# Kernel tuning notes

Hardware: AMD Instinct MI355X
Metric: run time of the kernel (lower is better)

## Reference

```python
import jax, jax.numpy as jnp
import numpy as np

THRESHOLD = 1.0  # CIF firing threshold (init kwarg)


def setup_inputs() -> dict:
    key = jax.random.key(0)
    k1, k2 = jax.random.split(key)
    B, T, H = 32, 2048, 512
    return {
        "hidden": jax.random.normal(k1, (B, T, H), dtype=jnp.float32),
        "alphas": jax.random.uniform(k2, (B, T), dtype=jnp.float32),
        "integrate": jnp.zeros((B,), dtype=jnp.float32),
        "frame": jnp.zeros((B, H), dtype=jnp.float32),
    }


def cif_scan(hidden, alphas, integrate, frame, threshold):
    """Continuous integrate-and-fire recurrence over time, vectorized over batch.

    hidden: [B,T,H], alphas: [B,T], integrate: [B], frame: [B,H]
    Returns fires [B,T], frames [B,T,H], integrate_new [B], frame_new [B,H].
    """

    def step(carry, inp):
        integ, fr = carry          # [B], [B,H]
        alpha, h_t = inp           # [B], [B,H]
        dist_completion = 1.0 - integ
        integ = integ + alpha
        fire = integ >= threshold                       # [B] bool
        integ_next = jnp.where(fire, integ - 1.0, integ)
        cur = jnp.where(fire, dist_completion, alpha)   # weight spent this step
        rem = alpha - cur                               # leftover weight after firing
        fr_out = fr + cur[:, None] * h_t                # frame recorded at this step
        fr_next = jnp.where(fire[:, None], rem[:, None] * h_t, fr_out)
        return (integ_next, fr_next), (integ, fr_out)

    xs = (jnp.swapaxes(alphas, 0, 1), jnp.swapaxes(hidden, 0, 1))  # time-major
    (integ_f, frame_f), (fires_t, frames_t) = jax.lax.scan(step, (integrate, frame), xs)
    fires = jnp.swapaxes(fires_t, 0, 1)    # [B,T]
    frames = jnp.swapaxes(frames_t, 0, 1)  # [B,T,H]
    return fires, frames, integ_f, frame_f


def reference(hidden, alphas, integrate, frame):
    T = hidden.shape[1]
    fires, frames, integ_new, frame_new = cif_scan(hidden, alphas, integrate, frame, THRESHOLD)
    # torch.index_select(frames[0], 0, nonzero(fires[0] >= threshold)) -> data-dependent
    # shape; emulate with jit-safe padded nonzero (padding rows replicate row 0).
    idx = jnp.nonzero(fires[0] >= THRESHOLD, size=T, fill_value=0)[0]
    frame_sel = frames[0][idx]  # [T, H], first num_fires rows are the fired frames
    return frame_sel, integ_new, frame_new
```

## Files before the change

### kernel.cpp

```cpp
#include <hip/hip_runtime.h>


#define THRESH 1.0f
#define MAX_T 4096
#define MAX_CH 64

__device__ __forceinline__ float fract_exact(float x) {
    float r; asm("v_fract_f32 %0, %1" : "=v"(r) : "v"(x)); return r;
}

__global__ __launch_bounds__(256) void cif_transpose_kernel(
    const float4* __restrict__ a4, float4* __restrict__ aT4, int B, int T4)
{
    int tid = blockIdx.x * blockDim.x + threadIdx.x;
    if (tid >= B * T4) return;
    int b = tid / T4, c = tid - b * T4;
    aT4[(size_t)c * B + b] = a4[tid];
}

__global__ __launch_bounds__(64) void cif_chain_kernel(
    const float4* __restrict__ aT4,
    const float*  __restrict__ integ0,
    float* __restrict__ chunkInteg,
    float* __restrict__ integ_out,
    int B, int T)
{
    const int lane = threadIdx.x;
    const bool act = lane < B;
    const int nchunk = T >> 6;
    float integ = act ? integ0[lane] : 0.0f;
    float4 bufA[16], bufB[16];

#define LOADCH(buf, c) do { if (act) { \
    _Pragma("unroll") for (int j = 0; j < 16; ++j) \
        buf[j] = aT4[(size_t)((c) * 16 + j) * B + lane]; } } while (0)

#define DOCH(buf, c) do { if (act) { \
    chunkInteg[(size_t)(c) * B + lane] = integ; \
    _Pragma("unroll") for (int j = 0; j < 16; ++j) { \
        integ = fract_exact(integ + buf[j].x); \
        integ = fract_exact(integ + buf[j].y); \
        integ = fract_exact(integ + buf[j].z); \
        integ = fract_exact(integ + buf[j].w); \
    } } } while (0)

    LOADCH(bufA, 0);
    for (int c = 0; c < nchunk; c += 2) {
        if (c + 1 < nchunk) LOADCH(bufB, c + 1);
        DOCH(bufA, c);
        if (c + 2 < nchunk) LOADCH(bufA, c + 2);
        if (c + 1 < nchunk) DOCH(bufB, c + 1);
    }
#undef LOADCH
#undef DOCH

    if (act) integ_out[lane] = integ;
}

__global__ __launch_bounds__(1024) void cif_replay_kernel(
    const float4* __restrict__ aT4,
    const float*  __restrict__ chunkInteg,
    float* __restrict__ gT,
    int* __restrict__ rowStart, int* __restrict__ rowEnd, int* __restrict__ rowFlags,
    int* __restrict__ tlast,
    int B, int T)
{
    const int nchunk = T >> 6;
    const int tid = threadIdx.x;
    __shared__ unsigned long long s_mask[2048];
    __shared__ int s_fire[MAX_T];
    __shared__ int s_nf, s_f0;

    if (tid < nchunk * B) {
        const int c = tid / B, b = tid - c * B;
        float integ = chunkInteg[tid];
        unsigned long long m = 0;
        for (int j = 0; j < 16; ++j) {
            const float4 a4 = aT4[(size_t)(c * 16 + j) * B + b];
            const float av[4] = {a4.x, a4.y, a4.z, a4.w};
            float gv[4];
#pragma unroll
            for (int k = 0; k < 4; ++k) {
                const int idx = j * 4 + k;
                const float alpha = av[k];
                const float s   = integ + alpha;
                const bool fire = (s >= THRESH);
                const float sm1 = s - 1.0f;
                integ = fire ? sm1 : s;
                gv[k] = fire ? sm1 : alpha;
                m |= fire ? (1ull << idx) : 0ull;
            }
#pragma unroll
            for (int k = 0; k < 4; ++k)
                gT[(size_t)(c * 64 + j * 4 + k) * B + b] = gv[k];
        }
        s_mask[tid] = m;
    }
    __syncthreads();

    if (tid < B) {
        int tl = -1;
        for (int c = nchunk - 1; c >= 0; --c) {
            const unsigned long long mc = s_mask[c * B + tid];
            if (mc) { tl = c * 64 + 63 - __clzll(mc); break; }
        }
        tlast[tid] = tl;
    }

    if (tid < 64) {
        unsigned long long m0 = (tid < nchunk) ? s_mask[tid * B] : 0ull;
        const int pc = __popcll(m0);
        int x = pc;
#pragma unroll
        for (int d = 1; d < 64; d <<= 1) {
            const int y = __shfl_up(x, d);
            if (tid >= d) x += y;
        }
        if (tid == 63) s_nf = x;
        if (tid == 0)  s_f0 = (int)(m0 & 1ull);
        int r = x - pc;
        while (m0) {
            const int p = __ffsll(m0) - 1;
            s_fire[r++] = tid * 64 + p;
            m0 &= m0 - 1;
        }
    }
    __syncthreads();

    const int nf = s_nf, f0 = s_f0;
    for (int r = tid; r < T; r += blockDim.x) {
        int st, en, fl;
        if (r < nf) {
            en = s_fire[r];
            st = (r == 0) ? 0 : s_fire[r - 1];
            fl = ((r == 0) ? 1 : 0) | 2;
        } else {
            st = 0; en = 0; fl = 1 | (f0 ? 2 : 0);
        }
        rowStart[r] = st; rowEnd[r] = en; rowFlags[r] = fl;
    }
}

__global__ __launch_bounds__(128) void cif_out_kernel(
    const float* __restrict__ hidden,
    const float* __restrict__ frame0,
    const float* __restrict__ gT,
    const float* __restrict__ alphas,
    const int* __restrict__ rowStart, const int* __restrict__ rowEnd,
    const int* __restrict__ rowFlags, const int* __restrict__ tlast,
    float* __restrict__ out_sel,
    float* __restrict__ frame_out,
    int B, int T, int H)
{
    const int blk = blockIdx.x;

    if (blk < T) {
        const int r = blk;
        const int start = rowStart[r], end = rowEnd[r], fl = rowFlags[r];
        const float a  = alphas[end];
        const float ge = gT[(size_t)end * B];
        const float wend = (fl & 2) ? (a - ge) : a;
        for (int h0 = threadIdx.x * 4; h0 < H; h0 += 128 * 4) {
            float4 acc = (fl & 1) ? *reinterpret_cast<const float4*>(frame0 + h0)
                                  : make_float4(0.f, 0.f, 0.f, 0.f);
            for (int s = start; s < end; ++s) {
                const float  w  = gT[(size_t)s * B];
                const float4 hv = *reinterpret_cast<const float4*>(hidden + (size_t)s * H + h0);
                acc.x += w * hv.x; acc.y += w * hv.y;
                acc.z += w * hv.z; acc.w += w * hv.w;
            }
            const float4 hv = *reinterpret_cast<const float4*>(hidden + (size_t)end * H + h0);
            acc.x += wend * hv.x; acc.y += wend * hv.y;
            acc.z += wend * hv.z; acc.w += wend * hv.w;
            *reinterpret_cast<float4*>(out_sel + (size_t)r * H + h0) = acc;
        }
    } else {
        const int b  = blk - T;
        const int tl = tlast[b];
        const int start = (tl < 0) ? 0 : tl;
        const float* hb = hidden + (size_t)b * T * H;
        for (int h0 = threadIdx.x * 4; h0 < H; h0 += 128 * 4) {
            float4 acc = (tl < 0) ? *reinterpret_cast<const float4*>(frame0 + (size_t)b * H + h0)
                                  : make_float4(0.f, 0.f, 0.f, 0.f);
            for (int s = start; s < T; ++s) {
                const float  w  = gT[(size_t)s * B + b];
                const float4 hv = *reinterpret_cast<const float4*>(hb + (size_t)s * H + h0);
                acc.x += w * hv.x; acc.y += w * hv.y;
                acc.z += w * hv.z; acc.w += w * hv.w;
            }
            *reinterpret_cast<float4*>(frame_out + (size_t)b * H + h0) = acc;
        }
    }
}

extern "C" void kernel_launch(void* const* d_in, const int* in_sizes, int n_in,
                              void* d_out, int out_size, void* d_ws, size_t ws_size,
                              hipStream_t stream) {
    const float* hidden    = (const float*)d_in[0];
    const float* alphas    = (const float*)d_in[1];
    const float* integrate = (const float*)d_in[2];
    const float* frame     = (const float*)d_in[3];

    const int B = in_sizes[2];
    const int T = in_sizes[1] / B;
    const int H = in_sizes[3] / B;

    float* out       = (float*)d_out;
    float* out_sel   = out;
    float* integ_out = out + (size_t)T * H;
    float* frame_out = integ_out + B;

    char* ws = (char*)d_ws;
    float4* aT4       = (float4*)ws;  ws += sizeof(float) * (size_t)B * T;
    float*  gT        = (float*)ws;   ws += sizeof(float) * (size_t)B * T;
    float*  chunkInteg= (float*)ws;   ws += sizeof(float) * (size_t)(T / 64) * B;
    int* rowStart = (int*)ws;         ws += sizeof(int) * T;
    int* rowEnd   = (int*)ws;         ws += sizeof(int) * T;
    int* rowFlags = (int*)ws;         ws += sizeof(int) * T;
    int* tlast    = (int*)ws;         ws += sizeof(int) * B;

    const int T4 = T / 4;
    cif_transpose_kernel<<<(B * T4 + 255) / 256, 256, 0, stream>>>(
        (const float4*)alphas, aT4, B, T4);

    cif_chain_kernel<<<1, 64, 0, stream>>>(
        aT4, integrate, chunkInteg, integ_out, B, T);

    cif_replay_kernel<<<1, 1024, 0, stream>>>(
        aT4, chunkInteg, gT, rowStart, rowEnd, rowFlags, tlast, B, T);

    cif_out_kernel<<<T + B, 128, 0, stream>>>(
        hidden, frame, gT, alphas, rowStart, rowEnd, rowFlags, tlast,
        out_sel, frame_out, B, T, H);
}
```

Baseline: 206.8 us.

## Fuse transpose, chain and replay kernels into one single-block prep kernel

Merges the alpha transpose, the chunk-level integrate chain and the per-chunk replay into one 512-thread single-block kernel. Chunk start values now stay in shared memory instead of a global buffer. This removes two kernel launches and their inter-kernel gaps. In exchange, the transpose that previously ran across many blocks is now done by a single block, and the replay loop runs with 512 threads instead of 1024, so it needs two passes.

```diff
diff --git a/kernel.cpp b/kernel.cpp
--- a/kernel.cpp
+++ b/kernel.cpp
@@ -2,82 +2,78 @@
 
 
 #define THRESH 1.0f
-#define MAX_T 4096
-#define MAX_CH 64
+#define MAXB   64
+#define MAXT   2048
+#define MAXCH  (MAXT / 64)
 
 __device__ __forceinline__ float fract_exact(float x) {
     float r; asm("v_fract_f32 %0, %1" : "=v"(r) : "v"(x)); return r;
 }
 
-__global__ __launch_bounds__(256) void cif_transpose_kernel(
-    const float4* __restrict__ a4, float4* __restrict__ aT4, int B, int T4)
-{
-    int tid = blockIdx.x * blockDim.x + threadIdx.x;
-    if (tid >= B * T4) return;
-    int b = tid / T4, c = tid - b * T4;
-    aT4[(size_t)c * B + b] = a4[tid];
-}
-
-__global__ __launch_bounds__(64) void cif_chain_kernel(
-    const float4* __restrict__ aT4,
+__global__ __launch_bounds__(512) void cif_prep_kernel(
+    const float4* __restrict__ a4,
     const float*  __restrict__ integ0,
-    float* __restrict__ chunkInteg,
+    float4* __restrict__ aT4,
+    float*  __restrict__ gT,
+    int* __restrict__ rowStart, int* __restrict__ rowEnd, int* __restrict__ rowFlags,
+    int* __restrict__ tlast,
     float* __restrict__ integ_out,
     int B, int T)
 {
-    const int lane = threadIdx.x;
-    const bool act = lane < B;
+    const int tid = threadIdx.x;
+    const int T4 = T >> 2;
     const int nchunk = T >> 6;
-    float integ = act ? integ0[lane] : 0.0f;
-    float4 bufA[16], bufB[16];
+
+    __shared__ float              s_ci[MAXCH * MAXB];
+    __shared__ unsigned long long s_mask[MAXCH * MAXB];
+    __shared__ int                s_fire[MAXT];
+    __shared__ int                s_nf, s_f0;
+
+    for (int i = tid; i < B * T4; i += 512) {
+        const int b = i / T4, c = i - b * T4;
+        aT4[(size_t)c * B + b] = a4[i];
+    }
+    __syncthreads();
+
+    if (tid < 64) {
+        const int lane = tid;
+        const bool act = lane < B;
+        float integ = act ? integ0[lane] : 0.0f;
+        float4 bufA[16], bufB[16];
 
 #define LOADCH(buf, c) do { if (act) { \
-    _Pragma("unroll") for (int j = 0; j < 16; ++j) \
-        buf[j] = aT4[(size_t)((c) * 16 + j) * B + lane]; } } while (0)
+        _Pragma("unroll") for (int j = 0; j < 16; ++j) \
+            buf[j] = aT4[(size_t)((c) * 16 + j) * B + lane]; } } while (0)
 
 #define DOCH(buf, c) do { if (act) { \
-    chunkInteg[(size_t)(c) * B + lane] = integ; \
-    _Pragma("unroll") for (int j = 0; j < 16; ++j) { \
-        integ = fract_exact(integ + buf[j].x); \
-        integ = fract_exact(integ + buf[j].y); \
-        integ = fract_exact(integ + buf[j].z); \
-        integ = fract_exact(integ + buf[j].w); \
-    } } } while (0)
-
-    LOADCH(bufA, 0);
-    for (int c = 0; c < nchunk; c += 2) {
-        if (c + 1 < nchunk) LOADCH(bufB, c + 1);
-        DOCH(bufA, c);
-        if (c + 2 < nchunk) LOADCH(bufA, c + 2);
-        if (c + 1 < nchunk) DOCH(bufB, c + 1);
-    }
+        s_ci[(c) * B + lane] = integ; \
+        _Pragma("unroll") for (int j = 0; j < 16; ++j) { \
+            integ = fract_exact(integ + buf[j].x); \
+            integ = fract_exact(integ + buf[j].y); \
+            integ = fract_exact(integ + buf[j].z); \
+            integ = fract_exact(integ + buf[j].w); \
+        } } } while (0)
+
+        LOADCH(bufA, 0);
+        for (int c = 0; c < nchunk; c += 2) {
+            if (c + 1 < nchunk) LOADCH(bufB, c + 1);
+            DOCH(bufA, c);
+            if (c + 2 < nchunk) LOADCH(bufA, c + 2);
+            if (c + 1 < nchunk) DOCH(bufB, c + 1);
+        }
 #undef LOADCH
 #undef DOCH
-
-    if (act) integ_out[lane] = integ;
-}
-
-__global__ __launch_bounds__(1024) void cif_replay_kernel(
-    const float4* __restrict__ aT4,
-    const float*  __restrict__ chunkInteg,
-    float* __restrict__ gT,
-    int* __restrict__ rowStart, int* __restrict__ rowEnd, int* __restrict__ rowFlags,
-    int* __restrict__ tlast,
-    int B, int T)
-{
-    const int nchunk = T >> 6;
-    const int tid = threadIdx.x;
-    __shared__ unsigned long long s_mask[2048];
-    __shared__ int s_fire[MAX_T];
-    __shared__ int s_nf, s_f0;
-
-    if (tid < nchunk * B) {
-        const int c = tid / B, b = tid - c * B;
-        float integ = chunkInteg[tid];
+        if (act) integ_out[lane] = integ;
+    }
+    __syncthreads();
+
+    for (int w = tid; w < nchunk * B; w += 512) {
+        const int c = w / B, b = w - c * B;
+        float integ = s_ci[w];
         unsigned long long m = 0;
         for (int j = 0; j < 16; ++j) {
-            const float4 a4 = aT4[(size_t)(c * 16 + j) * B + b];
-            const float av[4] = {a4.x, a4.y, a4.z, a4.w};
+            const float4 av4 = aT4[(size_t)(c * 16 + j) * B + b];
+            const float av[4] = {av4.x, av4.y, av4.z, av4.w};
             float gv[4];
 #pragma unroll
             for (int k = 0; k < 4; ++k) {
@@ -94,7 +90,7 @@
             for (int k = 0; k < 4; ++k)
                 gT[(size_t)(c * 64 + j * 4 + k) * B + b] = gv[k];
         }
-        s_mask[tid] = m;
+        s_mask[w] = m;
     }
     __syncthreads();
 
@@ -106,7 +102,6 @@
         }
         tlast[tid] = tl;
     }
-
     if (tid < 64) {
         unsigned long long m0 = (tid < nchunk) ? s_mask[tid * B] : 0ull;
         const int pc = __popcll(m0);
@@ -128,7 +123,7 @@
     __syncthreads();
 
     const int nf = s_nf, f0 = s_f0;
-    for (int r = tid; r < T; r += blockDim.x) {
+    for (int r = tid; r < T; r += 512) {
         int st, en, fl;
         if (r < nf) {
             en = s_fire[r];
@@ -211,23 +206,16 @@
     float* frame_out = integ_out + B;
 
     char* ws = (char*)d_ws;
-    float4* aT4       = (float4*)ws;  ws += sizeof(float) * (size_t)B * T;
-    float*  gT        = (float*)ws;   ws += sizeof(float) * (size_t)B * T;
-    float*  chunkInteg= (float*)ws;   ws += sizeof(float) * (size_t)(T / 64) * B;
-    int* rowStart = (int*)ws;         ws += sizeof(int) * T;
-    int* rowEnd   = (int*)ws;         ws += sizeof(int) * T;
-    int* rowFlags = (int*)ws;         ws += sizeof(int) * T;
-    int* tlast    = (int*)ws;         ws += sizeof(int) * B;
-
-    const int T4 = T / 4;
-    cif_transpose_kernel<<<(B * T4 + 255) / 256, 256, 0, stream>>>(
-        (const float4*)alphas, aT4, B, T4);
-
-    cif_chain_kernel<<<1, 64, 0, stream>>>(
-        aT4, integrate, chunkInteg, integ_out, B, T);
-
-    cif_replay_kernel<<<1, 1024, 0, stream>>>(
-        aT4, chunkInteg, gT, rowStart, rowEnd, rowFlags, tlast, B, T);
+    float4* aT4   = (float4*)ws;  ws += sizeof(float) * (size_t)B * T;
+    float*  gT    = (float*)ws;   ws += sizeof(float) * (size_t)B * T;
+    int* rowStart = (int*)ws;     ws += sizeof(int) * T;
+    int* rowEnd   = (int*)ws;     ws += sizeof(int) * T;
+    int* rowFlags = (int*)ws;     ws += sizeof(int) * T;
+    int* tlast    = (int*)ws;     ws += sizeof(int) * B;
+
+    cif_prep_kernel<<<1, 512, 0, stream>>>(
+        (const float4*)alphas, integrate, aT4, gT,
+        rowStart, rowEnd, rowFlags, tlast, integ_out, B, T);
 
     cif_out_kernel<<<T + B, 128, 0, stream>>>(
         hidden, frame, gT, alphas, rowStart, rowEnd, rowFlags, tlast,
```

Measured after the change: 243.3 us. 17.7% more time.
